# Performance work log

Hardware: AMD Instinct MI355X
Metric: run time of the kernel (lower is better)

The kernel has to match this reference:

```python
import jax, jax.numpy as jnp
import numpy as np

N_NODES = 10000
N_EDGES = 320000
D_IN = 256
D_OUT = 256
NEG_SLOPE = 0.2


def setup_inputs() -> dict:
    key = jax.random.key(0)
    ks = jax.random.split(key, 8)
    feature = jax.random.normal(ks[0], (N_NODES, D_IN), dtype=jnp.float32)
    src = jax.random.randint(ks[1], (N_EDGES,), 0, N_NODES, dtype=jnp.int32)
    dst = jax.random.randint(ks[2], (N_EDGES,), 0, N_NODES, dtype=jnp.int32)
    # Xavier-ish scaled weights
    s = 1.0 / np.sqrt(D_IN)
    W_s = jax.random.normal(ks[3], (D_OUT, D_IN), dtype=jnp.float32) * s
    W_t = jax.random.normal(ks[4], (D_OUT, D_IN), dtype=jnp.float32) * s
    W_attn = jax.random.normal(ks[5], (1, D_OUT), dtype=jnp.float32) * (1.0 / np.sqrt(D_OUT))
    W_fc = jax.random.normal(ks[6], (D_OUT, D_IN), dtype=jnp.float32) * s
    b_fc = jnp.zeros((D_OUT,), dtype=jnp.float32)
    return {"feature": feature, "src": src, "dst": dst,
            "W_s": W_s, "W_t": W_t, "W_attn": W_attn,
            "W_fc": W_fc, "b_fc": b_fc}


def reference(feature, src, dst, W_s, W_t, W_attn, W_fc, b_fc):
    n = feature.shape[0]
    # Project at node level, then gather (same math as projecting gathered feats).
    proj_s = feature @ W_s.T          # [N, D_OUT]
    proj_t = feature @ W_t.T          # [N, D_OUT]
    # Edge attention logits: attn(LeakyReLU(h_dst + h_src))
    z = proj_s[src] + proj_t[dst]     # [E, D_OUT]
    z = jnp.where(z >= 0, z, NEG_SLOPE * z)
    e = (z @ W_attn.T)[:, 0]          # [E]
    # edge_softmax with norm_by='src': softmax over outgoing edges of each src node
    m = jax.ops.segment_max(e, src, num_segments=n)          # [N]
    m = jnp.where(jnp.isfinite(m), m, 0.0)                   # guard empty segments
    e_exp = jnp.exp(e - m[src])                               # [E]
    denom = jax.ops.segment_sum(e_exp, src, num_segments=n)  # [N]
    alpha = e_exp / denom[src]                                # [E]
    # message = src feature * alpha; reduce = sum at dst
    msg = feature[src] * alpha[:, None]                       # [E, D_IN]
    agg = jax.ops.segment_sum(msg, dst, num_segments=n)       # [N, D_IN]
    # final linear
    return agg @ W_fc.T + b_fc
```

## Files before the change

kernel.cpp:

```cpp
#include <hip/hip_runtime.h>
#include <math.h>

#define N_NODES 10000
#define N_EDGES 320000
#define D 256
#define NEG_SLOPE 0.2f
#define BCAP 96
#define BLOCK 256
#define NF4 (N_NODES * D / 4)
#define NW4 (256 * 256 / 4)
#define NTILE_M 157
#define NTILES (NTILE_M * 12)
#define FILL_BLOCKS ((N_EDGES + BLOCK - 1) / BLOCK)
#define APAD 264
#define CPAD 66

typedef unsigned short ushortT;
typedef __attribute__((ext_vector_type(8))) short bf16x8;
typedef __attribute__((ext_vector_type(4))) float f32x4;

__device__ __forceinline__ unsigned short f2bf(float f) {
  unsigned int u = __float_as_uint(f);
  u += 0x7FFFu + ((u >> 16) & 1u);
  return (unsigned short)(u >> 16);
}
__device__ __forceinline__ float bf2f(unsigned short u) {
  return __uint_as_float((unsigned int)u << 16);
}

__global__ void prep_kernel(const float* __restrict__ feat,
                            const float* __restrict__ Ws,
                            const float* __restrict__ Wt,
                            const float* __restrict__ Wfc,
                            ushortT* __restrict__ featb,
                            ushortT* __restrict__ Wcat,
                            int* __restrict__ cnt,
                            float* __restrict__ denom) {
  const int g = blockIdx.x * blockDim.x + threadIdx.x;
  if (g < NF4) {
    float4 v = ((const float4*)feat)[g];
    ushort4 u;
    u.x = f2bf(v.x); u.y = f2bf(v.y); u.z = f2bf(v.z); u.w = f2bf(v.w);
    ((ushort4*)featb)[g] = u;
    return;
  }
  const int gi = g - NF4;
  if (gi < 3 * NW4) {
    const float* W = (gi < NW4) ? Ws : ((gi < 2 * NW4) ? Wt : Wfc);
    const int off = gi - ((gi < NW4) ? 0 : ((gi < 2 * NW4) ? NW4 : 2 * NW4));
    float4 v = ((const float4*)W)[off];
    ushort4 u;
    u.x = f2bf(v.x); u.y = f2bf(v.y); u.z = f2bf(v.z); u.w = f2bf(v.w);
    ((ushort4*)Wcat)[gi] = u;
    return;
  }
  const int gn = gi - 3 * NW4;
  if (gn < N_NODES) {
    cnt[gn] = 0;
    denom[gn] = 0.f;
  }
}

__global__ __launch_bounds__(256, 2) void proj_fill_kernel(
    const ushortT* __restrict__ featb,
    const ushortT* __restrict__ Wcat,
    const int* __restrict__ src, const int* __restrict__ dst,
    int* __restrict__ cnt, int* __restrict__ src_b,
    ushortT* __restrict__ ps, ushortT* __restrict__ pt,
    ushortT* __restrict__ fcp) {
  __shared__ ushortT Als[64][APAD];
  __shared__ ushortT Bls[64][APAD];
  __shared__ ushortT Cls[64][CPAD];

  if (blockIdx.x < FILL_BLOCKS) {
    const int i = blockIdx.x * BLOCK + threadIdx.x;
    if (i < N_EDGES) {
      const int dn = dst[i];
      const int slot = atomicAdd(&cnt[dn], 1);
      if (slot < BCAP) src_b[dn * BCAP + slot] = src[i];
    }
    return;
  }
  const int p = blockIdx.x - FILL_BLOCKS;
  const int m0 = (p / 12) * 64;
  const int by = p % 12;
  ushortT* outp = (by < 4) ? ps : ((by < 8) ? pt : fcp);
  const int col0 = (by & 3) * 64;
  const int n0 = by * 64;

  const int tid = threadIdx.x;
  const int wave = tid >> 6;
  const int lane = tid & 63;
  const int quad = lane >> 4;
  const int l16 = lane & 15;

  const int m_base_t = (wave & 1) * 32;
  const int wn = wave >> 1;

  const int tr = tid >> 2;
  const int tk = (tid & 3) * 64;
  const int gr = m0 + tr;
  const int wr = n0 + tr;
  const bf16x8 zero8 = {0, 0, 0, 0, 0, 0, 0, 0};
  bf16x8 av[8], bv[8];
#pragma unroll
  for (int i = 0; i < 8; ++i)
    av[i] = (gr < N_NODES) ? *(const bf16x8*)(featb + (size_t)gr * D + tk + 8 * i) : zero8;
#pragma unroll
  for (int i = 0; i < 8; ++i)
    bv[i] = *(const bf16x8*)(Wcat + (size_t)wr * D + tk + 8 * i);
#pragma unroll
  for (int i = 0; i < 8; ++i) *(bf16x8*)&Als[tr][tk + 8 * i] = av[i];
#pragma unroll
  for (int i = 0; i < 8; ++i) *(bf16x8*)&Bls[tr][tk + 8 * i] = bv[i];
  __syncthreads();

  f32x4 acc[2][2];
#pragma unroll
  for (int i = 0; i < 2; ++i)
#pragma unroll
    for (int j = 0; j < 2; ++j) acc[i][j] = (f32x4){0.f, 0.f, 0.f, 0.f};

  const int ar0 = m_base_t + l16;
  const int br0 = wn * 32 + l16;
#pragma unroll
  for (int kk = 0; kk < 8; ++kk) {
    const int ko = kk * 32 + quad * 8;
    bf16x8 a0 = *(const bf16x8*)&Als[ar0][ko];
    bf16x8 a1 = *(const bf16x8*)&Als[ar0 + 16][ko];
    bf16x8 b0 = *(const bf16x8*)&Bls[br0][ko];
    bf16x8 b1 = *(const bf16x8*)&Bls[br0 + 16][ko];
    acc[0][0] = __builtin_amdgcn_mfma_f32_16x16x32_bf16(a0, b0, acc[0][0], 0, 0, 0);
    acc[0][1] = __builtin_amdgcn_mfma_f32_16x16x32_bf16(a0, b1, acc[0][1], 0, 0, 0);
    acc[1][0] = __builtin_amdgcn_mfma_f32_16x16x32_bf16(a1, b0, acc[1][0], 0, 0, 0);
    acc[1][1] = __builtin_amdgcn_mfma_f32_16x16x32_bf16(a1, b1, acc[1][1], 0, 0, 0);
  }

#pragma unroll
  for (int mi = 0; mi < 2; ++mi)
#pragma unroll
    for (int r = 0; r < 4; ++r) {
      const int row = m_base_t + mi * 16 + quad * 4 + r;
#pragma unroll
      for (int ni = 0; ni < 2; ++ni)
        Cls[row][wn * 32 + ni * 16 + l16] = f2bf(acc[mi][ni][r]);
    }
  __syncthreads();
#pragma unroll
  for (int it = 0; it < 2; ++it) {
    const int idx = tid + it * 256;
    const int row = idx >> 3;
    const int cc = (idx & 7) * 8;
    const int grow = m0 + row;
    if (grow < N_NODES)
      *(bf16x8*)(outp + (size_t)grow * D + col0 + cc) = *(const bf16x8*)&Cls[row][cc];
  }
}

__global__ __launch_bounds__(256) void logit_bucket_kernel(
    const ushortT* __restrict__ ps,
    const ushortT* __restrict__ pt,
    const int* __restrict__ cnt,
    const int* __restrict__ src_b,
    const float* __restrict__ Wattn,
    float* __restrict__ expv_b,
    float* __restrict__ denom) {
  const int n = blockIdx.x;
  const int cn = min(cnt[n], BCAP);
  if (cn == 0) return;
  const int wave = threadIdx.x >> 6;
  const int lane = threadIdx.x & 63;
  const int half = lane >> 5;
  const int l32 = lane & 31;
  const int grp = wave * 2 + half;
  const int base = n * BCAP;

  bf16x8 bu = *(const bf16x8*)(pt + (size_t)n * D + l32 * 8);
  float b[8], w[8];
  const float4 w0 = *(const float4*)(Wattn + l32 * 8);
  const float4 w1 = *(const float4*)(Wattn + l32 * 8 + 4);
  w[0] = w0.x; w[1] = w0.y; w[2] = w0.z; w[3] = w0.w;
  w[4] = w1.x; w[5] = w1.y; w[6] = w1.z; w[7] = w1.w;
#pragma unroll
  for (int i = 0; i < 8; ++i) b[i] = bf2f((unsigned short)bu[i]);

  int j = grp;
  for (; j + 24 < cn; j += 32) {
    const int s0 = src_b[base + j];
    const int s1 = src_b[base + j + 8];
    const int s2 = src_b[base + j + 16];
    const int s3 = src_b[base + j + 24];
    bf16x8 au0 = *(const bf16x8*)(ps + (size_t)s0 * D + l32 * 8);
    bf16x8 au1 = *(const bf16x8*)(ps + (size_t)s1 * D + l32 * 8);
    bf16x8 au2 = *(const bf16x8*)(ps + (size_t)s2 * D + l32 * 8);
    bf16x8 au3 = *(const bf16x8*)(ps + (size_t)s3 * D + l32 * 8);
    float sum0 = 0.f, sum1 = 0.f, sum2 = 0.f, sum3 = 0.f;
#pragma unroll
    for (int i = 0; i < 8; ++i) {
      float z0 = bf2f((unsigned short)au0[i]) + b[i];
      float z1 = bf2f((unsigned short)au1[i]) + b[i];
      float z2 = bf2f((unsigned short)au2[i]) + b[i];
      float z3 = bf2f((unsigned short)au3[i]) + b[i];
      z0 = fmaxf(z0, NEG_SLOPE * z0);
      z1 = fmaxf(z1, NEG_SLOPE * z1);
      z2 = fmaxf(z2, NEG_SLOPE * z2);
      z3 = fmaxf(z3, NEG_SLOPE * z3);
      sum0 = fmaf(w[i], z0, sum0);
      sum1 = fmaf(w[i], z1, sum1);
      sum2 = fmaf(w[i], z2, sum2);
      sum3 = fmaf(w[i], z3, sum3);
    }
#pragma unroll
    for (int off = 16; off > 0; off >>= 1) {
      sum0 += __shfl_down(sum0, off, 32);
      sum1 += __shfl_down(sum1, off, 32);
      sum2 += __shfl_down(sum2, off, 32);
      sum3 += __shfl_down(sum3, off, 32);
    }
    if (l32 == 0) {
      float ex0 = __expf(sum0), ex1 = __expf(sum1);
      float ex2 = __expf(sum2), ex3 = __expf(sum3);
      expv_b[base + j] = ex0;
      expv_b[base + j + 8] = ex1;
      expv_b[base + j + 16] = ex2;
      expv_b[base + j + 24] = ex3;
      atomicAdd(&denom[s0], ex0);
      atomicAdd(&denom[s1], ex1);
      atomicAdd(&denom[s2], ex2);
      atomicAdd(&denom[s3], ex3);
    }
  }
  for (; j < cn; j += 8) {
    const int s = src_b[base + j];
    bf16x8 au = *(const bf16x8*)(ps + (size_t)s * D + l32 * 8);
    float sum = 0.f;
#pragma unroll
    for (int i = 0; i < 8; ++i) {
      float z = bf2f((unsigned short)au[i]) + b[i];
      z = fmaxf(z, NEG_SLOPE * z);
      sum = fmaf(w[i], z, sum);
    }
#pragma unroll
    for (int off = 16; off > 0; off >>= 1) sum += __shfl_down(sum, off, 32);
    if (l32 == 0) {
      float ex = __expf(sum);
      expv_b[base + j] = ex;
      atomicAdd(&denom[s], ex);
    }
  }
}

__global__ __launch_bounds__(256) void prescale_kernel(
    const ushortT* __restrict__ fcp,
    const float* __restrict__ denom,
    ushortT* __restrict__ fcpsb) {
  const int n = blockIdx.x * 4 + (threadIdx.x >> 6);
  if (n >= N_NODES) return;
  const int t = threadIdx.x & 63;
  const float inv = 1.0f / denom[n];
  ushort4 v = ((const ushort4*)(fcp + (size_t)n * D))[t];
  ushort4 o;
  o.x = f2bf(bf2f(v.x) * inv);
  o.y = f2bf(bf2f(v.y) * inv);
  o.z = f2bf(bf2f(v.z) * inv);
  o.w = f2bf(bf2f(v.w) * inv);
  ((ushort4*)(fcpsb + (size_t)n * D))[t] = o;
}

__global__ __launch_bounds__(256) void gather_agg_kernel(
    const ushortT* __restrict__ fcpsb,
    const int* __restrict__ cnt,
    const int* __restrict__ src_b,
    const float* __restrict__ expv_b,
    const float* __restrict__ b_fc,
    float* __restrict__ out) {
  __shared__ float red[8][D];
  const int n = blockIdx.x;
  const int tid = threadIdx.x;
  const int wave = tid >> 6;
  const int lane = tid & 63;
  const int half = lane >> 5;
  const int l32 = lane & 31;
  const int grp = wave * 2 + half;
  const int cn = min(cnt[n], BCAP);
  const int base = n * BCAP;

  float acc[8];
#pragma unroll
  for (int i = 0; i < 8; ++i) acc[i] = 0.f;

  int j = grp;
  for (; j + 24 < cn; j += 32) {
    const int s0 = src_b[base + j];
    const int s1 = src_b[base + j + 8];
    const int s2 = src_b[base + j + 16];
    const int s3 = src_b[base + j + 24];
    const float a0 = expv_b[base + j];
    const float a1 = expv_b[base + j + 8];
    const float a2 = expv_b[base + j + 16];
    const float a3 = expv_b[base + j + 24];
    bf16x8 f0 = *(const bf16x8*)(fcpsb + (size_t)s0 * D + l32 * 8);
    bf16x8 f1 = *(const bf16x8*)(fcpsb + (size_t)s1 * D + l32 * 8);
    bf16x8 f2 = *(const bf16x8*)(fcpsb + (size_t)s2 * D + l32 * 8);
    bf16x8 f3 = *(const bf16x8*)(fcpsb + (size_t)s3 * D + l32 * 8);
#pragma unroll
    for (int i = 0; i < 8; ++i) {
      acc[i] = fmaf(a0, bf2f((unsigned short)f0[i]), acc[i]);
      acc[i] = fmaf(a1, bf2f((unsigned short)f1[i]), acc[i]);
      acc[i] = fmaf(a2, bf2f((unsigned short)f2[i]), acc[i]);
      acc[i] = fmaf(a3, bf2f((unsigned short)f3[i]), acc[i]);
    }
  }
  for (; j < cn; j += 8) {
    const int s = src_b[base + j];
    const float a = expv_b[base + j];
    bf16x8 fu = *(const bf16x8*)(fcpsb + (size_t)s * D + l32 * 8);
#pragma unroll
    for (int i = 0; i < 8; ++i)
      acc[i] = fmaf(a, bf2f((unsigned short)fu[i]), acc[i]);
  }
  *(float4*)&red[grp][l32 * 8] = make_float4(acc[0], acc[1], acc[2], acc[3]);
  *(float4*)&red[grp][l32 * 8 + 4] = make_float4(acc[4], acc[5], acc[6], acc[7]);
  __syncthreads();
  float o = b_fc[tid];
#pragma unroll
  for (int g = 0; g < 8; ++g) o += red[g][tid];
  out[(size_t)n * D + tid] = o;
}

extern "C" void kernel_launch(void* const* d_in, const int* in_sizes, int n_in,
                              void* d_out, int out_size, void* d_ws, size_t ws_size,
                              hipStream_t stream) {
  const float* feat  = (const float*)d_in[0];
  const int*   src   = (const int*)d_in[1];
  const int*   dst   = (const int*)d_in[2];
  const float* Ws    = (const float*)d_in[3];
  const float* Wt    = (const float*)d_in[4];
  const float* Wattn = (const float*)d_in[5];
  const float* Wfc   = (const float*)d_in[6];
  const float* bfc   = (const float*)d_in[7];
  float* out = (float*)d_out;

  ushortT* ps    = (ushortT*)d_ws;
  ushortT* pt    = ps + (size_t)N_NODES * D;
  ushortT* fcp   = pt + (size_t)N_NODES * D;
  ushortT* featb = fcp + (size_t)N_NODES * D;
  ushortT* Wcat  = featb + (size_t)N_NODES * D;
  float* expv_b  = (float*)(Wcat + (size_t)768 * 256);
  float* denom   = expv_b + (size_t)N_NODES * BCAP;
  int*   cnt     = (int*)(denom + N_NODES);
  int*   src_b   = cnt + N_NODES;
  ushortT* fcpsb = featb;

  const int prep_items = NF4 + 3 * NW4 + N_NODES;
  prep_kernel<<<(prep_items + BLOCK - 1) / BLOCK, BLOCK, 0, stream>>>(
      feat, Ws, Wt, Wfc, featb, Wcat, cnt, denom);
  proj_fill_kernel<<<FILL_BLOCKS + NTILES, BLOCK, 0, stream>>>(
      featb, Wcat, src, dst, cnt, src_b, ps, pt, fcp);
  logit_bucket_kernel<<<N_NODES, BLOCK, 0, stream>>>(ps, pt, cnt, src_b, Wattn, expv_b, denom);
  prescale_kernel<<<(N_NODES + 3) / 4, BLOCK, 0, stream>>>(fcp, denom, fcpsb);
  gather_agg_kernel<<<N_NODES, BLOCK, 0, stream>>>(fcpsb, cnt, src_b, expv_b, bfc, out);
}
```

Before: 171.9 us.

## Fold bf16 conversion into projection GEMM and denom scaling into gather

Removes the separate prep kernel by loading fp32 features and weights directly in the projection tile loader and converting them to bf16 while storing to LDS, with staggered store order. It also drops the prescale kernel and divides each edge's exp value by denom[src] inside the gather loop. The counters are now cleared with a memset. This saves two launches and a full write and reread of the converted feature and prescaled buffers. In exchange, each GEMM tile reads twice as many bytes from global memory, and the gather adds one scattered denom load and a divide per edge.

```diff
diff --git a/kernel.cpp b/kernel.cpp
--- a/kernel.cpp
+++ b/kernel.cpp
@@ -7,8 +7,6 @@
 #define NEG_SLOPE 0.2f
 #define BCAP 96
 #define BLOCK 256
-#define NF4 (N_NODES * D / 4)
-#define NW4 (256 * 256 / 4)
 #define NTILE_M 157
 #define NTILES (NTILE_M * 12)
 #define FILL_BLOCKS ((N_EDGES + BLOCK - 1) / BLOCK)
@@ -27,43 +25,17 @@
 __device__ __forceinline__ float bf2f(unsigned short u) {
   return __uint_as_float((unsigned int)u << 16);
 }
-
-__global__ void prep_kernel(const float* __restrict__ feat,
-                            const float* __restrict__ Ws,
-                            const float* __restrict__ Wt,
-                            const float* __restrict__ Wfc,
-                            ushortT* __restrict__ featb,
-                            ushortT* __restrict__ Wcat,
-                            int* __restrict__ cnt,
-                            float* __restrict__ denom) {
-  const int g = blockIdx.x * blockDim.x + threadIdx.x;
-  if (g < NF4) {
-    float4 v = ((const float4*)feat)[g];
-    ushort4 u;
-    u.x = f2bf(v.x); u.y = f2bf(v.y); u.z = f2bf(v.z); u.w = f2bf(v.w);
-    ((ushort4*)featb)[g] = u;
-    return;
-  }
-  const int gi = g - NF4;
-  if (gi < 3 * NW4) {
-    const float* W = (gi < NW4) ? Ws : ((gi < 2 * NW4) ? Wt : Wfc);
-    const int off = gi - ((gi < NW4) ? 0 : ((gi < 2 * NW4) ? NW4 : 2 * NW4));
-    float4 v = ((const float4*)W)[off];
-    ushort4 u;
-    u.x = f2bf(v.x); u.y = f2bf(v.y); u.z = f2bf(v.z); u.w = f2bf(v.w);
-    ((ushort4*)Wcat)[gi] = u;
-    return;
-  }
-  const int gn = gi - 3 * NW4;
-  if (gn < N_NODES) {
-    cnt[gn] = 0;
-    denom[gn] = 0.f;
-  }
+__device__ __forceinline__ ushort4 f4bf(float4 v) {
+  ushort4 u;
+  u.x = f2bf(v.x); u.y = f2bf(v.y); u.z = f2bf(v.z); u.w = f2bf(v.w);
+  return u;
 }
 
 __global__ __launch_bounds__(256, 2) void proj_fill_kernel(
-    const ushortT* __restrict__ featb,
-    const ushortT* __restrict__ Wcat,
+    const float* __restrict__ feat,
+    const float* __restrict__ Ws,
+    const float* __restrict__ Wt,
+    const float* __restrict__ Wfc,
     const int* __restrict__ src, const int* __restrict__ dst,
     int* __restrict__ cnt, int* __restrict__ src_b,
     ushortT* __restrict__ ps, ushortT* __restrict__ pt,
@@ -85,8 +57,8 @@
   const int m0 = (p / 12) * 64;
   const int by = p % 12;
   ushortT* outp = (by < 4) ? ps : ((by < 8) ? pt : fcp);
+  const float* Wsel = (by < 4) ? Ws : ((by < 8) ? Wt : Wfc);
   const int col0 = (by & 3) * 64;
-  const int n0 = by * 64;
 
   const int tid = threadIdx.x;
   const int wave = tid >> 6;
@@ -98,21 +70,30 @@
   const int wn = wave >> 1;
 
   const int tr = tid >> 2;
-  const int tk = (tid & 3) * 64;
+  const int tcol = (tid & 3) * 64;
   const int gr = m0 + tr;
-  const int wr = n0 + tr;
-  const bf16x8 zero8 = {0, 0, 0, 0, 0, 0, 0, 0};
-  bf16x8 av[8], bv[8];
-#pragma unroll
-  for (int i = 0; i < 8; ++i)
-    av[i] = (gr < N_NODES) ? *(const bf16x8*)(featb + (size_t)gr * D + tk + 8 * i) : zero8;
-#pragma unroll
-  for (int i = 0; i < 8; ++i)
-    bv[i] = *(const bf16x8*)(Wcat + (size_t)wr * D + tk + 8 * i);
-#pragma unroll
-  for (int i = 0; i < 8; ++i) *(bf16x8*)&Als[tr][tk + 8 * i] = av[i];
-#pragma unroll
-  for (int i = 0; i < 8; ++i) *(bf16x8*)&Bls[tr][tk + 8 * i] = bv[i];
+  const int wrow = col0 + tr;
+  const float4 zero4 = make_float4(0.f, 0.f, 0.f, 0.f);
+  const int ph = (tid & 3) * 4;
+
+  float4 av[16];
+#pragma unroll
+  for (int i = 0; i < 16; ++i)
+    av[i] = (gr < N_NODES) ? *(const float4*)(feat + (size_t)gr * D + tcol + 4 * i) : zero4;
+#pragma unroll
+  for (int i = 0; i < 16; ++i) {
+    const int ii = (i + ph) & 15;
+    *(ushort4*)&Als[tr][tcol + 4 * ii] = f4bf(av[ii]);
+  }
+  float4 bv[16];
+#pragma unroll
+  for (int i = 0; i < 16; ++i)
+    bv[i] = *(const float4*)(Wsel + (size_t)wrow * D + tcol + 4 * i);
+#pragma unroll
+  for (int i = 0; i < 16; ++i) {
+    const int ii = (i + ph) & 15;
+    *(ushort4*)&Bls[tr][tcol + 4 * ii] = f4bf(bv[ii]);
+  }
   __syncthreads();
 
   f32x4 acc[2][2];
@@ -250,28 +231,12 @@
   }
 }
 
-__global__ __launch_bounds__(256) void prescale_kernel(
+__global__ __launch_bounds__(256) void gather_agg_kernel(
     const ushortT* __restrict__ fcp,
-    const float* __restrict__ denom,
-    ushortT* __restrict__ fcpsb) {
-  const int n = blockIdx.x * 4 + (threadIdx.x >> 6);
-  if (n >= N_NODES) return;
-  const int t = threadIdx.x & 63;
-  const float inv = 1.0f / denom[n];
-  ushort4 v = ((const ushort4*)(fcp + (size_t)n * D))[t];
-  ushort4 o;
-  o.x = f2bf(bf2f(v.x) * inv);
-  o.y = f2bf(bf2f(v.y) * inv);
-  o.z = f2bf(bf2f(v.z) * inv);
-  o.w = f2bf(bf2f(v.w) * inv);
-  ((ushort4*)(fcpsb + (size_t)n * D))[t] = o;
-}
-
-__global__ __launch_bounds__(256) void gather_agg_kernel(
-    const ushortT* __restrict__ fcpsb,
     const int* __restrict__ cnt,
     const int* __restrict__ src_b,
     const float* __restrict__ expv_b,
+    const float* __restrict__ denom,
     const float* __restrict__ b_fc,
     float* __restrict__ out) {
   __shared__ float red[8][D];
@@ -295,14 +260,14 @@
     const int s1 = src_b[base + j + 8];
     const int s2 = src_b[base + j + 16];
     const int s3 = src_b[base + j + 24];
-    const float a0 = expv_b[base + j];
-    const float a1 = expv_b[base + j + 8];
-    const float a2 = expv_b[base + j + 16];
-    const float a3 = expv_b[base + j + 24];
-    bf16x8 f0 = *(const bf16x8*)(fcpsb + (size_t)s0 * D + l32 * 8);
-    bf16x8 f1 = *(const bf16x8*)(fcpsb + (size_t)s1 * D + l32 * 8);
-    bf16x8 f2 = *(const bf16x8*)(fcpsb + (size_t)s2 * D + l32 * 8);
-    bf16x8 f3 = *(const bf16x8*)(fcpsb + (size_t)s3 * D + l32 * 8);
+    const float a0 = expv_b[base + j] / denom[s0];
+    const float a1 = expv_b[base + j + 8] / denom[s1];
+    const float a2 = expv_b[base + j + 16] / denom[s2];
+    const float a3 = expv_b[base + j + 24] / denom[s3];
+    bf16x8 f0 = *(const bf16x8*)(fcp + (size_t)s0 * D + l32 * 8);
+    bf16x8 f1 = *(const bf16x8*)(fcp + (size_t)s1 * D + l32 * 8);
+    bf16x8 f2 = *(const bf16x8*)(fcp + (size_t)s2 * D + l32 * 8);
+    bf16x8 f3 = *(const bf16x8*)(fcp + (size_t)s3 * D + l32 * 8);
 #pragma unroll
     for (int i = 0; i < 8; ++i) {
       acc[i] = fmaf(a0, bf2f((unsigned short)f0[i]), acc[i]);
@@ -313,8 +278,8 @@
   }
   for (; j < cn; j += 8) {
     const int s = src_b[base + j];
-    const float a = expv_b[base + j];
-    bf16x8 fu = *(const bf16x8*)(fcpsb + (size_t)s * D + l32 * 8);
+    const float a = expv_b[base + j] / denom[s];
+    bf16x8 fu = *(const bf16x8*)(fcp + (size_t)s * D + l32 * 8);
 #pragma unroll
     for (int i = 0; i < 8; ++i)
       acc[i] = fmaf(a, bf2f((unsigned short)fu[i]), acc[i]);
@@ -344,20 +309,14 @@
   ushortT* ps    = (ushortT*)d_ws;
   ushortT* pt    = ps + (size_t)N_NODES * D;
   ushortT* fcp   = pt + (size_t)N_NODES * D;
-  ushortT* featb = fcp + (size_t)N_NODES * D;
-  ushortT* Wcat  = featb + (size_t)N_NODES * D;
-  float* expv_b  = (float*)(Wcat + (size_t)768 * 256);
+  float* expv_b  = (float*)(fcp + (size_t)N_NODES * D);
   float* denom   = expv_b + (size_t)N_NODES * BCAP;
   int*   cnt     = (int*)(denom + N_NODES);
   int*   src_b   = cnt + N_NODES;
-  ushortT* fcpsb = featb;
-
-  const int prep_items = NF4 + 3 * NW4 + N_NODES;
-  prep_kernel<<<(prep_items + BLOCK - 1) / BLOCK, BLOCK, 0, stream>>>(
-      feat, Ws, Wt, Wfc, featb, Wcat, cnt, denom);
+
+  hipMemsetAsync(denom, 0, N_NODES * (sizeof(float) + sizeof(int)), stream);
   proj_fill_kernel<<<FILL_BLOCKS + NTILES, BLOCK, 0, stream>>>(
-      featb, Wcat, src, dst, cnt, src_b, ps, pt, fcp);
+      feat, Ws, Wt, Wfc, src, dst, cnt, src_b, ps, pt, fcp);
   logit_bucket_kernel<<<N_NODES, BLOCK, 0, stream>>>(ps, pt, cnt, src_b, Wattn, expv_b, denom);
-  prescale_kernel<<<(N_NODES + 3) / 4, BLOCK, 0, stream>>>(fcp, denom, fcpsb);
-  gather_agg_kernel<<<N_NODES, BLOCK, 0, stream>>>(fcpsb, cnt, src_b, expv_b, bfc, out);
-}
+  gather_agg_kernel<<<N_NODES, BLOCK, 0, stream>>>(fcp, cnt, src_b, expv_b, denom, bfc, out);
+}
```

Measured after the change: 298.5 us. +73.7%, slower.
